# Performance work log

Hardware: AMD Instinct MI355X
Metric: run time of the kernel (lower is better)

The kernel has to match this reference:

```python
import jax, jax.numpy as jnp
import numpy as np

N, C_IN, C_OUT, L, V, P, K, STRIDE = 8, 256, 256, 512, 25, 3, 9, 1
BN_EPS = 1e-5


def setup_inputs() -> dict:
    key = jax.random.key(0)
    k1, k2, k3, k4, k5 = jax.random.split(key, 5)
    x = jax.random.normal(k1, (N, C_IN, L, V), dtype=jnp.float32)
    # 1x1 Conv2d weight, no bias: (out_channels*num_partitions, in_channels)
    conv_w = jax.random.normal(k2, (C_OUT * P, C_IN), dtype=jnp.float32) * (1.0 / np.sqrt(C_IN))
    # adjacency (P, V, V)
    A = jax.random.normal(k3, (P, V, V), dtype=jnp.float32) * 0.2
    bn_gamma = jnp.ones((C_OUT,), dtype=jnp.float32)
    bn_beta = jnp.zeros((C_OUT,), dtype=jnp.float32)
    bn_mean = jax.random.normal(k4, (C_OUT,), dtype=jnp.float32) * 0.1
    bn_var = jax.random.uniform(k5, (C_OUT,), dtype=jnp.float32) + 0.5
    return {"x": x, "conv_w": conv_w, "A": A, "bn_gamma": bn_gamma,
            "bn_beta": bn_beta, "bn_mean": bn_mean, "bn_var": bn_var}


def reference(x, conv_w, A, bn_gamma, bn_beta, bn_mean, bn_var):
    # residual branch: identity (in_channels == out_channels, stride == 1)
    res = x
    # 1x1 conv: (N, C_in, L, V) -> (N, C_out*P, L, V)
    y = jnp.einsum('nclv,oc->nolv', x, conv_w)
    # split channels into P partitions, stack, permute -> (N, L, P, C_out, V)
    y = y.reshape(N, P, C_OUT, L, V).transpose(0, 3, 1, 2, 4)
    # graph aggregation: x @ A per partition
    y = jnp.einsum('nlpcv,pvw->nlpcw', y, A)
    # sum over partitions -> (N, L, C_out, V)
    s = y.sum(axis=2)
    # FIFO with zero init + strided taps == causal strided window sum:
    # out[t] = sum_{k=0}^{K-1} s[t - k*STRIDE], zero-padded for t-k*STRIDE < 0
    pad = (K - 1) * STRIDE
    s_pad = jnp.pad(s, ((0, 0), (pad, 0), (0, 0), (0, 0)))
    out = s_pad[:, 0:L]
    for k in range(1, K):
        out = out + s_pad[:, k * STRIDE:k * STRIDE + L]
    # stack along dim 2 in torch -> (N, C_out, L, V)
    out = out.transpose(0, 2, 1, 3)
    # BatchNorm2d (eval, running stats) + ReLU
    scale = bn_gamma * jax.lax.rsqrt(bn_var + BN_EPS)
    shift = bn_beta - bn_mean * scale
    out = out * scale[None, :, None, None] + shift[None, :, None, None]
    out = jax.nn.relu(out)
    # residual add, then ReLU (Dropout p=0.0 is identity)
    out = jax.nn.relu(out + res)
    return out
```

## Files before the change

kernel.cpp:

```cpp
#include <hip/hip_runtime.h>
#include <hip/hip_bf16.h>

#define NB 8
#define CC 256
#define OO 768
#define LL 512
#define VV 25
#define PP 3
#define KM 768
#define NKC 24
#define LT 2

typedef __attribute__((ext_vector_type(8))) short short8v;
typedef __attribute__((ext_vector_type(4))) float float4v;
typedef __attribute__((ext_vector_type(4))) int int4v;

__device__ inline unsigned pk2(float a, float b){
    __hip_bfloat16 ha = __float2bfloat16(a), hb = __float2bfloat16(b);
    unsigned short ua = *(unsigned short*)&ha, ub = *(unsigned short*)&hb;
    return (unsigned)ua | ((unsigned)ub << 16);
}

__global__ __launch_bounds__(256) void wperm_kernel(const float* __restrict__ W,
                                                    __hip_bfloat16* __restrict__ Wp) {
    int idx = blockIdx.x * 256 + threadIdx.x;
    if (idx >= OO * CC) return;
    int j    = idx & 7;
    int lane = (idx >> 3) & 63;
    int mt   = (idx >> 9) & 3;
    int wm   = (idx >> 11) & 3;
    int kc   = idx >> 13;
    int c = wm * 64 + mt * 16 + (lane & 15);
    int k = kc * 32 + ((lane >> 4) << 3) + j;
    int cib = k / 192;
    int r = k - cib * 192;
    int p = r >> 6;
    int ci = cib * 64 + (r & 63);
    Wp[idx] = __float2bfloat16(W[(p * 256 + c) * 256 + ci]);
}

__global__ __launch_bounds__(256, 4) void fused_main_kernel(
    const float* __restrict__ x,
    const __hip_bfloat16* __restrict__ Wp,
    const float* __restrict__ A,
    const float* __restrict__ gamma, const float* __restrict__ beta,
    const float* __restrict__ mean, const float* __restrict__ var,
    float* __restrict__ out)
{
    __shared__ __hip_bfloat16 Zb[2][64 * 32];
    __shared__ __hip_bfloat16 xsh[128 * 32];
    __shared__ __hip_bfloat16 a2t[3 * 32 * 32];
    __shared__ float scsh[512];

    const int tid  = threadIdx.x;
    const int lane = tid & 63, wid = tid >> 6;
    const int lcol = lane & 15, grp = lane >> 4;
    const int bid0 = blockIdx.x;
    const int swz = (bid0 & 7) * 256 + (bid0 >> 3);
    const int n  = swz >> 8;
    const int l0 = (swz & 255) * LT;
    const int wm = wid;
    const int mt_z = wid & 1, l_z = wid >> 1;

    {
        int4v z = {0, 0, 0, 0};
        ((int4v*)xsh)[tid] = z;
        ((int4v*)xsh)[tid + 256] = z;
        ((int4v*)a2t)[tid] = z;
        if (tid < 128) ((int4v*)a2t)[tid + 256] = z;
        float sc = gamma[tid] * rsqrtf(var[tid] + 1e-5f);
        scsh[tid] = sc;
        scsh[256 + tid] = beta[tid] - mean[tid] * sc;
    }
    __syncthreads();
    for (int idx = tid; idx < PP * VV * VV; idx += 256) {
        int p = idx / 625, r = idx - p * 625, v = r / 25, w = r - v * 25;
        int R = p * 32 + w;
        int e = (((v >> 3) ^ ((R >> 1) & 3)) << 3) | (v & 7);
        a2t[R * 32 + e] = __float2bfloat16(A[idx]);
    }

    auto stage_xs = [&](int cib) {
        for (int cc = tid; cc < 1600; cc += 256) {
            int ci6 = cc / 25, v = cc - ci6 * 25;
            const float* xp = x + ((size_t)(n * CC + cib * 64 + ci6) * LL) * VV + v;
            float rbuf[10];
            #pragma unroll
            for (int j = 0; j < 10; ++j) {
                int lj = l0 - 8 + j;
                rbuf[j] = (lj >= 0) ? xp[(size_t)lj * VV] : 0.f;
            }
            float wsv = 0.f;
            #pragma unroll
            for (int j = 0; j < 9; ++j) wsv += rbuf[j];
            #pragma unroll
            for (int i = 0; i < LT; ++i) {
                int R = ci6 * LT + i;
                int e = (((v >> 3) ^ ((R >> 1) & 3)) << 3) | (v & 7);
                xsh[R * 32 + e] = __float2bfloat16(wsv);
                if (i < LT - 1) wsv += rbuf[9 + i] - rbuf[i];
            }
        }
    };
    auto zgen = [&](int kc, int zbuf) {
        int p = (kc % 6) >> 1, h = kc & 1;
        int ci6 = h * 32 + mt_z * 16 + lcol;
        int R = ci6 * LT + l_z;
        short8v az = *(const short8v*)&xsh[R * 32 + ((grp ^ ((R >> 1) & 3)) << 3)];
        #pragma unroll
        for (int wt = 0; wt < 2; ++wt) {
            int R2 = p * 32 + wt * 16 + lcol;
            short8v bz = *(const short8v*)&a2t[R2 * 32 + ((grp ^ ((R2 >> 1) & 3)) << 3)];
            float4v zc = {0.f, 0.f, 0.f, 0.f};
            zc = __builtin_amdgcn_mfma_f32_16x16x32_bf16(az, bz, zc, 0, 0, 0);
            int R3 = l_z * 32 + wt * 16 + lcol;
            int eb = (mt_z * 2 + (grp >> 1)) ^ ((R3 >> 1) & 3);
            unsigned* dst = (unsigned*)&Zb[zbuf][R3 * 32 + (eb << 3) + ((grp & 1) << 2)];
            dst[0] = pk2(zc[0], zc[1]);
            dst[1] = pk2(zc[2], zc[3]);
        }
    };

    float4v acc[4][4];
    #pragma unroll
    for (int i = 0; i < 4; ++i)
        #pragma unroll
        for (int j = 0; j < 4; ++j) acc[i][j] = (float4v){0.f, 0.f, 0.f, 0.f};

    const __hip_bfloat16* afbase = Wp + ((size_t)(wm * 4) * 64 + lane) * 8;

#define KSTEP(kc, j, afc, afn) do {                                           \
    if ((kc) + 1 < NKC) {                                                     \
        const __hip_bfloat16* ap_ = afbase + (size_t)((kc) + 1) * 8192;       \
        _Pragma("unroll")                                                     \
        for (int mt_ = 0; mt_ < 4; ++mt_)                                     \
            afn[mt_] = *(const short8v*)(ap_ + mt_ * 512);                    \
    }                                                                         \
    if ((j) < 5) zgen((kc) + 1, ((kc) + 1) & 1);                              \
    {                                                                         \
        const __hip_bfloat16* zcur_ = &Zb[(kc) & 1][0];                       \
        short8v bf_[4];                                                       \
        _Pragma("unroll")                                                     \
        for (int nt_ = 0; nt_ < 4; ++nt_) {                                   \
            int R3_ = nt_ * 16 + lcol;                                        \
            bf_[nt_] = *(const short8v*)&zcur_[R3_ * 32 + ((grp ^ ((R3_ >> 1) & 3)) << 3)]; \
        }                                                                     \
        _Pragma("unroll")                                                     \
        for (int mt_ = 0; mt_ < 4; ++mt_)                                     \
            _Pragma("unroll")                                                 \
            for (int nt_ = 0; nt_ < 4; ++nt_)                                 \
                acc[mt_][nt_] = __builtin_amdgcn_mfma_f32_16x16x32_bf16(afc[mt_], bf_[nt_], acc[mt_][nt_], 0, 0, 0); \
    }                                                                         \
    asm volatile("s_waitcnt lgkmcnt(0)" ::: "memory");                        \
    __builtin_amdgcn_sched_barrier(0);                                        \
    __builtin_amdgcn_s_barrier();                                             \
} while (0)

    short8v afA[4], afB[4];
    #pragma unroll
    for (int mt = 0; mt < 4; ++mt) afA[mt] = *(const short8v*)(afbase + mt * 512);

    #pragma unroll 1
    for (int cib = 0; cib < 4; ++cib) {
        stage_xs(cib);
        asm volatile("s_waitcnt lgkmcnt(0)" ::: "memory");
        __builtin_amdgcn_sched_barrier(0);
        __builtin_amdgcn_s_barrier();

        zgen(cib * 6, (cib * 6) & 1);
        asm volatile("s_waitcnt lgkmcnt(0)" ::: "memory");
        __builtin_amdgcn_sched_barrier(0);
        __builtin_amdgcn_s_barrier();

        #pragma unroll 1
        for (int jj = 0; jj < 3; ++jj) {
            KSTEP(cib * 6 + jj * 2,     jj * 2,     afA, afB);
            KSTEP(cib * 6 + jj * 2 + 1, jj * 2 + 1, afB, afA);
        }
    }
#undef KSTEP

    #pragma unroll
    for (int mt = 0; mt < 4; ++mt) {
        #pragma unroll
        for (int nt = 0; nt < 4; ++nt) {
            int lw = nt * 16;
            int w = lw & 31;
            int l = l0 + (lw >> 5);
            int wl = w + lcol;
            if (wl < VV) {
                #pragma unroll
                for (int r = 0; r < 4; ++r) {
                    int c = wm * 64 + mt * 16 + grp * 4 + r;
                    float val = fmaf(acc[mt][nt][r], scsh[c], scsh[256 + c]);
                    val = fmaxf(val, 0.f);
                    size_t ad = ((size_t)(n * CC + c) * LL + l) * VV + wl;
                    val = fmaxf(val + x[ad], 0.f);
                    out[ad] = val;
                }
            }
        }
    }
}

__global__ __launch_bounds__(256) void wsum_kernel(const float* __restrict__ x,
                                                   float* __restrict__ xs) {
    const int CHUNKS = 8;
    int t = blockIdx.x * 256 + threadIdx.x;
    if (t >= NB * CC * VV * CHUNKS) return;
    int v = t % VV;
    int r = t / VV;
    int chunk = r % CHUNKS;
    int nc = r / CHUNKS;
    int l0 = chunk * (LL / CHUNKS);
    const float* xp = x  + (size_t)nc * (LL * VV) + v;
    float*       op = xs + (size_t)nc * (LL * VV) + v;
    float ring[8];
    float run = 0.f;
    #pragma unroll
    for (int k = 0; k < 8; ++k) {
        int j = l0 - 8 + k;
        float val = (j >= 0) ? xp[j * VV] : 0.f;
        ring[k] = val; run += val;
    }
    for (int base = l0; base < l0 + LL / CHUNKS; base += 8) {
        #pragma unroll
        for (int k = 0; k < 8; ++k) {
            int l = base + k;
            float val = xp[l * VV];
            float o = run + val;
            op[l * VV] = o;
            run = o - ring[k];
            ring[k] = val;
        }
    }
}

__global__ __launch_bounds__(256) void fused_fallback_kernel(
    const float* xs, const float* __restrict__ x, const float* __restrict__ W,
    const float* __restrict__ A,
    const float* __restrict__ gamma, const float* __restrict__ beta,
    const float* __restrict__ mean, const float* __restrict__ var,
    float* out)
{
    __shared__ float xshf[CC][28];
    const int bid = blockIdx.x;
    const int n = bid >> 9;
    const int l = bid & 511;
    const int tid = threadIdx.x;
    const size_t nbase = (size_t)n * CC * LL * VV;
    for (int k = tid; k < CC * VV; k += 256) {
        int ci = k / VV, v = k - ci * VV;
        xshf[ci][v] = xs[nbase + (size_t)ci * (LL * VV) + (size_t)l * VV + v];
    }
    __syncthreads();
    const int c = tid;
    float Y[PP * VV];
    #pragma unroll
    for (int i = 0; i < PP * VV; ++i) Y[i] = 0.f;
    const float* Wpr = W + c * 256;
    #pragma unroll 1
    for (int ci = 0; ci < CC; ++ci) {
        float xv[VV];
        #pragma unroll
        for (int v = 0; v < VV; ++v) xv[v] = xshf[ci][v];
        float w0 = Wpr[ci], w1 = Wpr[65536 + ci], w2 = Wpr[131072 + ci];
        #pragma unroll
        for (int v = 0; v < VV; ++v) Y[v]          = fmaf(w0, xv[v], Y[v]);
        #pragma unroll
        for (int v = 0; v < VV; ++v) Y[VV + v]     = fmaf(w1, xv[v], Y[VV + v]);
        #pragma unroll
        for (int v = 0; v < VV; ++v) Y[2 * VV + v] = fmaf(w2, xv[v], Y[2 * VV + v]);
    }
    float o[VV];
    #pragma unroll
    for (int w = 0; w < VV; ++w) o[w] = 0.f;
    #pragma unroll
    for (int p = 0; p < PP; ++p)
        #pragma unroll
        for (int v = 0; v < VV; ++v) {
            float y = Y[p * VV + v];
            const float* Ap = A + (p * VV + v) * VV;
            #pragma unroll
            for (int w = 0; w < VV; ++w) o[w] = fmaf(y, Ap[w], o[w]);
        }
    float sc = gamma[c] * rsqrtf(var[c] + 1e-5f);
    float sh = beta[c] - mean[c] * sc;
    const float* resp = x   + nbase + (size_t)c * (LL * VV) + (size_t)l * VV;
    float*       outp = out + nbase + (size_t)c * (LL * VV) + (size_t)l * VV;
    #pragma unroll
    for (int w = 0; w < VV; ++w) {
        float t2 = fmaf(o[w], sc, sh);
        t2 = fmaxf(t2, 0.f);
        t2 = fmaxf(t2 + resp[w], 0.f);
        outp[w] = t2;
    }
}

extern "C" void kernel_launch(void* const* d_in, const int* in_sizes, int n_in,
                              void* d_out, int out_size, void* d_ws, size_t ws_size,
                              hipStream_t stream) {
    const float* x  = (const float*)d_in[0];
    const float* W  = (const float*)d_in[1];
    const float* A  = (const float*)d_in[2];
    const float* gm = (const float*)d_in[3];
    const float* bt = (const float*)d_in[4];
    const float* mn = (const float*)d_in[5];
    const float* vr = (const float*)d_in[6];
    float* out = (float*)d_out;

    if (ws_size >= (size_t)(OO * CC * sizeof(__hip_bfloat16))) {
        __hip_bfloat16* Wp = (__hip_bfloat16*)d_ws;
        wperm_kernel<<<dim3((OO * CC + 255) / 256), dim3(256), 0, stream>>>(W, Wp);
        fused_main_kernel<<<dim3(NB * (LL / LT)), dim3(256), 0, stream>>>(
            x, Wp, A, gm, bt, mn, vr, out);
    } else {
        const int threadsA = NB * CC * VV * 8;
        wsum_kernel<<<dim3((threadsA + 255) / 256), dim3(256), 0, stream>>>(x, out);
        fused_fallback_kernel<<<dim3(NB * LL), dim3(256), 0, stream>>>(
            out, x, W, A, gm, bt, mn, vr, out);
    }
}
```

Baseline: 115.1 us.

## Compute graph-aggregated Z tile per wave redundantly to remove per-step block barriers

Each wave now computes the full Z tile (x window-sum times A) into its own private LDS buffer instead of the four waves splitting the work and sharing a double-buffered Z. This removes the block-wide barrier after every K-step, leaving only two barriers per input-channel block, and it drops the register prefetch of the next weight fragments. It also adds s_setprio around the MFMA burst. The cost is four times the redundant Z-generation MFMAs and LDS writes, plus loss of the explicit overlap of weight loads with compute.

```diff
diff --git a/kernel.cpp b/kernel.cpp
--- a/kernel.cpp
+++ b/kernel.cpp
@@ -14,6 +14,7 @@
 typedef __attribute__((ext_vector_type(8))) short short8v;
 typedef __attribute__((ext_vector_type(4))) float float4v;
 typedef __attribute__((ext_vector_type(4))) int int4v;
+typedef __attribute__((ext_vector_type(2))) unsigned uint2v;
 
 __device__ inline unsigned pk2(float a, float b){
     __hip_bfloat16 ha = __float2bfloat16(a), hb = __float2bfloat16(b);
@@ -47,7 +48,7 @@
     const float* __restrict__ mean, const float* __restrict__ var,
     float* __restrict__ out)
 {
-    __shared__ __hip_bfloat16 Zb[2][64 * 32];
+    __shared__ __hip_bfloat16 Zp[4][64 * 32];
     __shared__ __hip_bfloat16 xsh[128 * 32];
     __shared__ __hip_bfloat16 a2t[3 * 32 * 32];
     __shared__ float scsh[512];
@@ -60,7 +61,6 @@
     const int n  = swz >> 8;
     const int l0 = (swz & 255) * LT;
     const int wm = wid;
-    const int mt_z = wid & 1, l_z = wid >> 1;
 
     {
         int4v z = {0, 0, 0, 0};
@@ -95,31 +95,13 @@
             for (int j = 0; j < 9; ++j) wsv += rbuf[j];
             #pragma unroll
             for (int i = 0; i < LT; ++i) {
-                int R = ci6 * LT + i;
+                int R = i * 64 + ci6;
                 int e = (((v >> 3) ^ ((R >> 1) & 3)) << 3) | (v & 7);
                 xsh[R * 32 + e] = __float2bfloat16(wsv);
                 if (i < LT - 1) wsv += rbuf[9 + i] - rbuf[i];
             }
         }
     };
-    auto zgen = [&](int kc, int zbuf) {
-        int p = (kc % 6) >> 1, h = kc & 1;
-        int ci6 = h * 32 + mt_z * 16 + lcol;
-        int R = ci6 * LT + l_z;
-        short8v az = *(const short8v*)&xsh[R * 32 + ((grp ^ ((R >> 1) & 3)) << 3)];
-        #pragma unroll
-        for (int wt = 0; wt < 2; ++wt) {
-            int R2 = p * 32 + wt * 16 + lcol;
-            short8v bz = *(const short8v*)&a2t[R2 * 32 + ((grp ^ ((R2 >> 1) & 3)) << 3)];
-            float4v zc = {0.f, 0.f, 0.f, 0.f};
-            zc = __builtin_amdgcn_mfma_f32_16x16x32_bf16(az, bz, zc, 0, 0, 0);
-            int R3 = l_z * 32 + wt * 16 + lcol;
-            int eb = (mt_z * 2 + (grp >> 1)) ^ ((R3 >> 1) & 3);
-            unsigned* dst = (unsigned*)&Zb[zbuf][R3 * 32 + (eb << 3) + ((grp & 1) << 2)];
-            dst[0] = pk2(zc[0], zc[1]);
-            dst[1] = pk2(zc[2], zc[3]);
-        }
-    };
 
     float4v acc[4][4];
     #pragma unroll
@@ -128,57 +110,72 @@
         for (int j = 0; j < 4; ++j) acc[i][j] = (float4v){0.f, 0.f, 0.f, 0.f};
 
     const __hip_bfloat16* afbase = Wp + ((size_t)(wm * 4) * 64 + lane) * 8;
-
-#define KSTEP(kc, j, afc, afn) do {                                           \
-    if ((kc) + 1 < NKC) {                                                     \
-        const __hip_bfloat16* ap_ = afbase + (size_t)((kc) + 1) * 8192;       \
-        _Pragma("unroll")                                                     \
-        for (int mt_ = 0; mt_ < 4; ++mt_)                                     \
-            afn[mt_] = *(const short8v*)(ap_ + mt_ * 512);                    \
-    }                                                                         \
-    if ((j) < 5) zgen((kc) + 1, ((kc) + 1) & 1);                              \
-    {                                                                         \
-        const __hip_bfloat16* zcur_ = &Zb[(kc) & 1][0];                       \
-        short8v bf_[4];                                                       \
-        _Pragma("unroll")                                                     \
-        for (int nt_ = 0; nt_ < 4; ++nt_) {                                   \
-            int R3_ = nt_ * 16 + lcol;                                        \
-            bf_[nt_] = *(const short8v*)&zcur_[R3_ * 32 + ((grp ^ ((R3_ >> 1) & 3)) << 3)]; \
-        }                                                                     \
-        _Pragma("unroll")                                                     \
-        for (int mt_ = 0; mt_ < 4; ++mt_)                                     \
-            _Pragma("unroll")                                                 \
-            for (int nt_ = 0; nt_ < 4; ++nt_)                                 \
-                acc[mt_][nt_] = __builtin_amdgcn_mfma_f32_16x16x32_bf16(afc[mt_], bf_[nt_], acc[mt_][nt_], 0, 0, 0); \
-    }                                                                         \
-    asm volatile("s_waitcnt lgkmcnt(0)" ::: "memory");                        \
-    __builtin_amdgcn_sched_barrier(0);                                        \
-    __builtin_amdgcn_s_barrier();                                             \
-} while (0)
-
-    short8v afA[4], afB[4];
-    #pragma unroll
-    for (int mt = 0; mt < 4; ++mt) afA[mt] = *(const short8v*)(afbase + mt * 512);
+    __hip_bfloat16* zp = &Zp[wid][0];
 
     #pragma unroll 1
     for (int cib = 0; cib < 4; ++cib) {
+        __syncthreads();
         stage_xs(cib);
-        asm volatile("s_waitcnt lgkmcnt(0)" ::: "memory");
-        __builtin_amdgcn_sched_barrier(0);
-        __builtin_amdgcn_s_barrier();
-
-        zgen(cib * 6, (cib * 6) & 1);
-        asm volatile("s_waitcnt lgkmcnt(0)" ::: "memory");
-        __builtin_amdgcn_sched_barrier(0);
-        __builtin_amdgcn_s_barrier();
+        __syncthreads();
 
         #pragma unroll 1
-        for (int jj = 0; jj < 3; ++jj) {
-            KSTEP(cib * 6 + jj * 2,     jj * 2,     afA, afB);
-            KSTEP(cib * 6 + jj * 2 + 1, jj * 2 + 1, afB, afA);
-        }
-    }
-#undef KSTEP
+        for (int j = 0; j < 6; ++j) {
+            const int kc = cib * 6 + j;
+            const int p = j >> 1, h = j & 1;
+
+            short8v af[4];
+            {
+                const __hip_bfloat16* ap = afbase + (size_t)kc * 8192;
+                #pragma unroll
+                for (int mt = 0; mt < 4; ++mt)
+                    af[mt] = *(const short8v*)(ap + mt * 512);
+            }
+
+            short8v bz[2];
+            #pragma unroll
+            for (int wt = 0; wt < 2; ++wt) {
+                int R2 = p * 32 + wt * 16 + lcol;
+                bz[wt] = *(const short8v*)&a2t[R2 * 32 + ((grp ^ ((R2 >> 1) & 3)) << 3)];
+            }
+            #pragma unroll
+            for (int l = 0; l < 2; ++l) {
+                short8v az[2];
+                #pragma unroll
+                for (int ks = 0; ks < 2; ++ks) {
+                    int R = l * 64 + h * 32 + ks * 16 + lcol;
+                    az[ks] = *(const short8v*)&xsh[R * 32 + ((grp ^ ((R >> 1) & 3)) << 3)];
+                }
+                #pragma unroll
+                for (int wt = 0; wt < 2; ++wt) {
+                    #pragma unroll
+                    for (int ks = 0; ks < 2; ++ks) {
+                        float4v zc = {0.f, 0.f, 0.f, 0.f};
+                        zc = __builtin_amdgcn_mfma_f32_16x16x32_bf16(az[ks], bz[wt], zc, 0, 0, 0);
+                        int R3 = l * 32 + wt * 16 + lcol;
+                        int kblk = ks * 2 + (grp >> 1);
+                        int e = ((kblk ^ ((R3 >> 1) & 3)) << 3) + ((grp & 1) << 2);
+                        uint2v u; u.x = pk2(zc[0], zc[1]); u.y = pk2(zc[2], zc[3]);
+                        *(uint2v*)&zp[R3 * 32 + e] = u;
+                    }
+                }
+            }
+
+            short8v bf[4];
+            #pragma unroll
+            for (int nt = 0; nt < 4; ++nt) {
+                int R3 = nt * 16 + lcol;
+                bf[nt] = *(const short8v*)&zp[R3 * 32 + ((grp ^ ((R3 >> 1) & 3)) << 3)];
+            }
+
+            __builtin_amdgcn_s_setprio(1);
+            #pragma unroll
+            for (int mt = 0; mt < 4; ++mt)
+                #pragma unroll
+                for (int nt = 0; nt < 4; ++nt)
+                    acc[mt][nt] = __builtin_amdgcn_mfma_f32_16x16x32_bf16(af[mt], bf[nt], acc[mt][nt], 0, 0, 0);
+            __builtin_amdgcn_s_setprio(0);
+        }
+    }
 
     #pragma unroll
     for (int mt = 0; mt < 4; ++mt) {
```

New measurement: 127.3 us. 10.6% more time.
